# Kernel tuning notes

Hardware: AMD Instinct MI355X
Metric: run time of the kernel (lower is better)

## Reference

```python
import jax, jax.numpy as jnp
import numpy as np

N_GROUPS = 10000
T = 0.07
EPS = 1e-12  # matches torch F.normalize default eps


def setup_inputs() -> dict:
    key = jax.random.key(0)
    k1, k2, k3, k4, k5 = jax.random.split(key, 5)
    B, D, N = 4096, 128, 500000
    x = jax.random.normal(k1, (B, D), dtype=jnp.float32)
    x_index = jax.random.randint(k2, (B,), 0, N, dtype=jnp.int64)
    y = jax.random.randint(k3, (B,), 0, N_GROUPS, dtype=jnp.int64)
    memory = jax.random.normal(k4, (N, D), dtype=jnp.float32)
    # normalize memory rows like a real memory bank
    memory = memory / jnp.linalg.norm(memory, axis=1, keepdims=True)
    group_ids = jax.random.randint(k5, (N,), 0, N_GROUPS, dtype=jnp.int64)
    return {"x": x, "x_index": x_index, "y": y, "memory": memory, "group_ids": group_ids}


def reference(x, x_index, y, memory, group_ids):
    # Segmented mean over memory rows per inv_map group (vectorized form of the
    # python loop: vi[k] = normalize(memory[inv_map[k]].mean(axis=0))).
    sums = jax.ops.segment_sum(memory, group_ids, num_segments=N_GROUPS)  # [G, D]
    counts = jax.ops.segment_sum(jnp.ones((memory.shape[0],), memory.dtype),
                                 group_ids, num_segments=N_GROUPS)        # [G]
    mean = sums / jnp.maximum(counts, 1.0)[:, None]                       # [G, D]
    norm = jnp.linalg.norm(mean, axis=1, keepdims=True)
    vi = mean / jnp.maximum(norm, EPS)                                    # [G, D]
    out = (x @ vi.T) / T                                                  # [B, G]
    return out
```

## Files before the change

kernel.cpp:

```cpp
#include <hip/hip_runtime.h>
#include <hip/hip_bf16.h>

#define GG 10000
#define DD 128

typedef __bf16 bf16x8 __attribute__((ext_vector_type(8)));
typedef float  f32x4  __attribute__((ext_vector_type(4)));

#define GLDS(src, dst) __builtin_amdgcn_global_load_lds( \
    (const __attribute__((address_space(1))) void*)(src), \
    (__attribute__((address_space(3))) void*)(dst), 16, 0, 0)


__global__ void k_zero(int* __restrict__ counts) {
    int i = blockIdx.x * blockDim.x + threadIdx.x;
    if (i < GG) counts[i] = 0;
}

__global__ void k_hist(const int* __restrict__ gid, int* __restrict__ counts,
                       int n4, int n) {
    int i = blockIdx.x * blockDim.x + threadIdx.x;
    if (i < n4) {
        int4 v = ((const int4*)gid)[i];
        atomicAdd(&counts[v.x], 1);
        atomicAdd(&counts[v.y], 1);
        atomicAdd(&counts[v.z], 1);
        atomicAdd(&counts[v.w], 1);
    }
    if (i == 0) {
        for (int r = n4 * 4; r < n; ++r) atomicAdd(&counts[gid[r]], 1);
    }
}

__global__ void k_scan(const int* __restrict__ counts, int* __restrict__ offsets,
                       int* __restrict__ cursor) {
    __shared__ int part[256];
    const int PER = 40;
    int t = threadIdx.x;
    int base = t * PER;
    int local[PER];
    int s = 0;
#pragma unroll
    for (int i = 0; i < PER; ++i) {
        int idx = base + i;
        int c = (idx < GG) ? counts[idx] : 0;
        local[i] = s;
        s += c;
    }
    part[t] = s;
    __syncthreads();
    for (int off = 1; off < 256; off <<= 1) {
        int v = part[t];
        int add = (t >= off) ? part[t - off] : 0;
        __syncthreads();
        part[t] = v + add;
        __syncthreads();
    }
    int cb = (t > 0) ? part[t - 1] : 0;
#pragma unroll
    for (int i = 0; i < PER; ++i) {
        int idx = base + i;
        if (idx < GG) {
            int o = cb + local[i];
            offsets[idx] = o;
            cursor[idx]  = o;
        }
    }
}

__global__ void k_scatter(const int* __restrict__ gid, int* __restrict__ cursor,
                          int* __restrict__ row_idx, int n4, int n) {
    int i = blockIdx.x * blockDim.x + threadIdx.x;
    if (i < n4) {
        int4 v = ((const int4*)gid)[i];
        int b = i * 4;
        row_idx[atomicAdd(&cursor[v.x], 1)] = b + 0;
        row_idx[atomicAdd(&cursor[v.y], 1)] = b + 1;
        row_idx[atomicAdd(&cursor[v.z], 1)] = b + 2;
        row_idx[atomicAdd(&cursor[v.w], 1)] = b + 3;
    }
    if (i == 0) {
        for (int r = n4 * 4; r < n; ++r)
            row_idx[atomicAdd(&cursor[gid[r]], 1)] = r;
    }
}

__global__ __launch_bounds__(256) void k_group_mean(
    const float* __restrict__ mem, const int* __restrict__ row_idx,
    const int* __restrict__ offsets, const int* __restrict__ counts,
    __bf16* __restrict__ vhi, __bf16* __restrict__ vlo) {
    int g = blockIdx.x;
    int t = threadIdx.x;
    int d = t & 127;
    int h = t >> 7;
    int off = offsets[g], cnt = counts[g];
    int half = cnt >> 1;
    int r    = h ? half : 0;
    int rend = h ? cnt  : half;
    float s = 0.f;
    for (; r + 4 <= rend; r += 4) {
        int i0 = row_idx[off + r + 0];
        int i1 = row_idx[off + r + 1];
        int i2 = row_idx[off + r + 2];
        int i3 = row_idx[off + r + 3];
        float a0 = mem[(size_t)i0 * DD + d];
        float a1 = mem[(size_t)i1 * DD + d];
        float a2 = mem[(size_t)i2 * DD + d];
        float a3 = mem[(size_t)i3 * DD + d];
        s += (a0 + a1) + (a2 + a3);
    }
    for (; r < rend; ++r) s += mem[(size_t)row_idx[off + r] * DD + d];

    __shared__ float part[128];
    if (h) part[d] = s;
    __syncthreads();
    float stot = h ? 0.f : (s + part[d]);
    float sq = stot * stot;
#pragma unroll
    for (int m = 32; m >= 1; m >>= 1) sq += __shfl_xor(sq, m);
    __shared__ float red[4];
    if ((t & 63) == 0) red[t >> 6] = sq;
    __syncthreads();
    float ss = red[0] + red[1] + red[2] + red[3];
    if (h == 0) {
        float scale = (ss > 0.f) ? rsqrtf(ss) : 0.f;
        float v = stot * scale;
        __bf16 hi = (__bf16)v;
        vhi[(size_t)g * DD + d] = hi;
        vlo[(size_t)g * DD + d] = (__bf16)(v - (float)hi);
    }
}

__global__ void k_prep_x(const float* __restrict__ x, __bf16* __restrict__ xhi,
                         __bf16* __restrict__ xlo, int n8) {
    int i = blockIdx.x * blockDim.x + threadIdx.x;
    if (i < n8) {
        float4 a = ((const float4*)x)[i * 2];
        float4 b = ((const float4*)x)[i * 2 + 1];
        float va[8] = {a.x, a.y, a.z, a.w, b.x, b.y, b.z, b.w};
        bf16x8 hv, lv;
#pragma unroll
        for (int j = 0; j < 8; ++j) {
            __bf16 hh = (__bf16)va[j];
            hv[j] = hh;
            lv[j] = (__bf16)(va[j] - (float)hh);
        }
        ((bf16x8*)xhi)[i] = hv;
        ((bf16x8*)xlo)[i] = lv;
    }
}

__global__ __launch_bounds__(256) void k_gemm(
    const __bf16* __restrict__ xhi, const __bf16* __restrict__ xlo,
    const __bf16* __restrict__ vhi, const __bf16* __restrict__ vlo,
    float* __restrict__ out) {
    __shared__ __bf16 sAh[128 * 64], sAl[128 * 64], sBh[128 * 64], sBl[128 * 64];
    const int t = threadIdx.x;
    const int lane = t & 63;
    const int w = t >> 6;
    const int wr = w >> 1, wc = w & 1;
    const int l16 = lane & 15, l4 = lane >> 4;
    const int rowTile = blockIdx.x * 128;
    const int colTile = blockIdx.y * 128;

    const int lrow = lane >> 3;
    const int lcol = lane & 7;
    const int srcCol = ((lcol ^ lrow) << 3);

    f32x4 acc[4][4] = {};

    for (int ks = 0; ks < 2; ++ks) {
        const int k0 = ks * 64;
#pragma unroll
        for (int tt = 0; tt < 4; ++tt) {
            const int rloc = w * 32 + tt * 8;
            const int arow = rowTile + rloc + lrow;
            int bcol = colTile + rloc + lrow;
            if (bcol >= GG) bcol = GG - 1;
            const size_t ao = (size_t)arow * DD + k0 + srcCol;
            const size_t bo = (size_t)bcol * DD + k0 + srcCol;
            GLDS(xhi + ao, &sAh[rloc * 64]);
            GLDS(xlo + ao, &sAl[rloc * 64]);
            GLDS(vhi + bo, &sBh[rloc * 64]);
            GLDS(vlo + bo, &sBl[rloc * 64]);
        }
        __syncthreads();

#pragma unroll
        for (int kk = 0; kk < 2; ++kk) {
            bf16x8 ah[4], al[4], bh[4], bl[4];
#pragma unroll
            for (int i = 0; i < 4; ++i) {
                const int Ra = wr * 64 + i * 16 + l16;
                const int ab = Ra * 128 + (((l4 << 4) + (kk << 6)) ^ ((Ra & 7) << 4));
                ah[i] = *(const bf16x8*)((const char*)sAh + ab);
                al[i] = *(const bf16x8*)((const char*)sAl + ab);
                const int Rb = wc * 64 + i * 16 + l16;
                const int bb = Rb * 128 + (((l4 << 4) + (kk << 6)) ^ ((Rb & 7) << 4));
                bh[i] = *(const bf16x8*)((const char*)sBh + bb);
                bl[i] = *(const bf16x8*)((const char*)sBl + bb);
            }
#pragma unroll
            for (int i = 0; i < 4; ++i)
#pragma unroll
                for (int j = 0; j < 4; ++j) {
                    acc[i][j] = __builtin_amdgcn_mfma_f32_16x16x32_bf16(ah[i], bh[j], acc[i][j], 0, 0, 0);
                    acc[i][j] = __builtin_amdgcn_mfma_f32_16x16x32_bf16(ah[i], bl[j], acc[i][j], 0, 0, 0);
                    acc[i][j] = __builtin_amdgcn_mfma_f32_16x16x32_bf16(al[i], bh[j], acc[i][j], 0, 0, 0);
                }
        }
        __syncthreads();
    }

    const float invT = 1.0f / 0.07f;
#pragma unroll
    for (int i = 0; i < 4; ++i) {
        const int row = rowTile + wr * 64 + i * 16 + l4 * 4;
#pragma unroll
        for (int j = 0; j < 4; ++j) {
            const int col = colTile + wc * 64 + j * 16 + l16;
            if (col < GG) {
#pragma unroll
                for (int r2 = 0; r2 < 4; ++r2)
                    out[(size_t)(row + r2) * GG + col] = acc[i][j][r2] * invT;
            }
        }
    }
}

extern "C" void kernel_launch(void* const* d_in, const int* in_sizes, int n_in,
                              void* d_out, int out_size, void* d_ws, size_t ws_size,
                              hipStream_t stream) {
    const float* x      = (const float*)d_in[0];
    const float* memory = (const float*)d_in[3];
    const int*   gid    = (const int*)d_in[4];

    int B = in_sizes[0] / DD;
    int N = in_sizes[4];

    char* ws = (char*)d_ws;
    int* counts  = (int*)(ws + 0);
    int* offsets = (int*)(ws + 40960);
    int* cursor  = (int*)(ws + 81920);
    int* row_idx = (int*)(ws + 122880);
    size_t o = 122880 + (size_t)N * 4;
    o = (o + 255) & ~(size_t)255;
    __bf16* xhi = (__bf16*)(ws + o);  o += (size_t)B * DD * 2;
    __bf16* xlo = (__bf16*)(ws + o);  o += (size_t)B * DD * 2;
    __bf16* vhi = (__bf16*)(ws + o);  o += (size_t)GG * DD * 2;
    __bf16* vlo = (__bf16*)(ws + o);  o += (size_t)GG * DD * 2;
    (void)ws_size; (void)n_in; (void)out_size;

    int n4 = N / 4;
    k_zero<<<(GG + 255) / 256, 256, 0, stream>>>(counts);
    k_hist<<<(n4 + 255) / 256, 256, 0, stream>>>(gid, counts, n4, N);
    k_scan<<<1, 256, 0, stream>>>(counts, offsets, cursor);
    k_scatter<<<(n4 + 255) / 256, 256, 0, stream>>>(gid, cursor, row_idx, n4, N);
    k_group_mean<<<GG, 256, 0, stream>>>(memory, row_idx, offsets, counts, vhi, vlo);
    int n8 = B * DD / 8;
    k_prep_x<<<(n8 + 255) / 256, 256, 0, stream>>>(x, xhi, xlo, n8);
    dim3 ggrid(B / 128, (GG + 127) / 128);
    k_gemm<<<ggrid, 256, 0, stream>>>(xhi, xlo, vhi, vlo, (float*)d_out);
}
```

Measured before the change: 526.4 us.

## Vectorize group-mean gathers across 8 row groups and stage scan counts in LDS

The group-mean kernel now has each of 8 row-groups of 32 threads read whole memory rows as float4 vectors. The next row index is prefetched while the current row loads, and the partial sums are reduced through shared memory, replacing the two-half scalar-per-dimension scheme. The scan kernel loads counts into LDS with coalesced accesses and writes offsets back coalesced, instead of each thread touching a strided block of 40 entries. The goal is more memory-level parallelism and wider loads on the bandwidth-bound gather, at the cost of a larger shared-memory footprint in the scan.

Result: no change. 516.6 us (-1.9%).

```diff
diff --git a/kernel.cpp b/kernel.cpp
--- a/kernel.cpp
+++ b/kernel.cpp
@@ -5,6 +5,7 @@
 #define DD 128
 
 typedef __bf16 bf16x8 __attribute__((ext_vector_type(8)));
+typedef __bf16 bf16x4 __attribute__((ext_vector_type(4)));
 typedef float  f32x4  __attribute__((ext_vector_type(4)));
 
 #define GLDS(src, dst) __builtin_amdgcn_global_load_lds( \
@@ -32,19 +33,22 @@
     }
 }
 
-__global__ void k_scan(const int* __restrict__ counts, int* __restrict__ offsets,
-                       int* __restrict__ cursor) {
+__global__ __launch_bounds__(256) void k_scan(const int* __restrict__ counts,
+                                              int* __restrict__ offsets,
+                                              int* __restrict__ cursor) {
+    const int PER = 40;
+    __shared__ int lds[256 * PER];
     __shared__ int part[256];
-    const int PER = 40;
+    __shared__ int pbase[256];
     int t = threadIdx.x;
+    for (int i = t; i < 256 * PER; i += 256) lds[i] = (i < GG) ? counts[i] : 0;
+    __syncthreads();
     int base = t * PER;
-    int local[PER];
     int s = 0;
 #pragma unroll
     for (int i = 0; i < PER; ++i) {
-        int idx = base + i;
-        int c = (idx < GG) ? counts[idx] : 0;
-        local[i] = s;
+        int c = lds[base + i];
+        lds[base + i] = s;
         s += c;
     }
     part[t] = s;
@@ -56,15 +60,12 @@
         part[t] = v + add;
         __syncthreads();
     }
-    int cb = (t > 0) ? part[t - 1] : 0;
-#pragma unroll
-    for (int i = 0; i < PER; ++i) {
-        int idx = base + i;
-        if (idx < GG) {
-            int o = cb + local[i];
-            offsets[idx] = o;
-            cursor[idx]  = o;
-        }
+    pbase[t] = (t > 0) ? part[t - 1] : 0;
+    __syncthreads();
+    for (int i = t; i < GG; i += 256) {
+        int o = lds[i] + pbase[i / PER];
+        offsets[i] = o;
+        cursor[i]  = o;
     }
 }
 
@@ -91,43 +92,43 @@
     __bf16* __restrict__ vhi, __bf16* __restrict__ vlo) {
     int g = blockIdx.x;
     int t = threadIdx.x;
-    int d = t & 127;
-    int h = t >> 7;
+    int rg = t >> 5;
+    int dq = t & 31;
     int off = offsets[g], cnt = counts[g];
-    int half = cnt >> 1;
-    int r    = h ? half : 0;
-    int rend = h ? cnt  : half;
-    float s = 0.f;
-    for (; r + 4 <= rend; r += 4) {
-        int i0 = row_idx[off + r + 0];
-        int i1 = row_idx[off + r + 1];
-        int i2 = row_idx[off + r + 2];
-        int i3 = row_idx[off + r + 3];
-        float a0 = mem[(size_t)i0 * DD + d];
-        float a1 = mem[(size_t)i1 * DD + d];
-        float a2 = mem[(size_t)i2 * DD + d];
-        float a3 = mem[(size_t)i3 * DD + d];
-        s += (a0 + a1) + (a2 + a3);
-    }
-    for (; r < rend; ++r) s += mem[(size_t)row_idx[off + r] * DD + d];
-
-    __shared__ float part[128];
-    if (h) part[d] = s;
-    __syncthreads();
-    float stot = h ? 0.f : (s + part[d]);
-    float sq = stot * stot;
-#pragma unroll
-    for (int m = 32; m >= 1; m >>= 1) sq += __shfl_xor(sq, m);
-    __shared__ float red[4];
-    if ((t & 63) == 0) red[t >> 6] = sq;
-    __syncthreads();
-    float ss = red[0] + red[1] + red[2] + red[3];
-    if (h == 0) {
-        float scale = (ss > 0.f) ? rsqrtf(ss) : 0.f;
-        float v = stot * scale;
-        __bf16 hi = (__bf16)v;
-        vhi[(size_t)g * DD + d] = hi;
-        vlo[(size_t)g * DD + d] = (__bf16)(v - (float)hi);
+
+    f32x4 s = {0.f, 0.f, 0.f, 0.f};
+    int r = rg;
+    int idx = (r < cnt) ? row_idx[off + r] : 0;
+    while (r < cnt) {
+        int nr = r + 8;
+        int nidx = (nr < cnt) ? row_idx[off + nr] : 0;
+        f32x4 a = *(const f32x4*)(mem + (size_t)idx * DD + dq * 4);
+        s += a;
+        idx = nidx;
+        r = nr;
+    }
+
+    __shared__ f32x4 red[8][32];
+    red[rg][dq] = s;
+    __syncthreads();
+    if (t < 32) {
+        f32x4 tot = red[0][t];
+#pragma unroll
+        for (int i = 1; i < 8; ++i) tot += red[i][t];
+        float sq = tot[0]*tot[0] + tot[1]*tot[1] + tot[2]*tot[2] + tot[3]*tot[3];
+#pragma unroll
+        for (int m = 16; m >= 1; m >>= 1) sq += __shfl_xor(sq, m);
+        float scale = (sq > 0.f) ? rsqrtf(sq) : 0.f;
+        bf16x4 hv, lv;
+#pragma unroll
+        for (int j = 0; j < 4; ++j) {
+            float v = tot[j] * scale;
+            __bf16 hi = (__bf16)v;
+            hv[j] = hi;
+            lv[j] = (__bf16)(v - (float)hi);
+        }
+        *(bf16x4*)(vhi + (size_t)g * DD + t * 4) = hv;
+        *(bf16x4*)(vlo + (size_t)g * DD + t * 4) = lv;
     }
 }
 
```
